# Kernel optimization log

Hardware: AMD Instinct MI355X
Metric: run time of the kernel (lower is better)

## Reference

```python
import jax, jax.numpy as jnp
import numpy as np

N = 50000      # nodes
DEG = 32       # avg degree
E = N * DEG + N  # edges incl. self loops
IN_DIM = 512
H = 4          # heads
D = 128        # hidden per head
SLOPE = 0.2


def setup_inputs() -> dict:
    key = jax.random.key(0)
    ks = jax.random.split(key, 12)
    features = jax.random.normal(ks[0], (N, IN_DIM), dtype=jnp.float32)
    src_r = jax.random.randint(ks[1], (N * DEG,), 0, N)
    dst_r = jax.random.randint(ks[2], (N * DEG,), 0, N)
    loop = jnp.arange(N)
    src = jnp.concatenate([src_r, loop]).astype(jnp.int32)
    dst = jnp.concatenate([dst_r, loop]).astype(jnp.int32)
    ids = jax.random.randint(ks[3], (16,), 0, N)
    s0 = 1.0 / np.sqrt(IN_DIM)
    s1 = 1.0 / np.sqrt(H * D)
    fc_w0 = jax.random.normal(ks[4], (IN_DIM, H * D), dtype=jnp.float32) * s0
    attn_l0 = jax.random.normal(ks[5], (H, D), dtype=jnp.float32) * s1
    attn_r0 = jax.random.normal(ks[6], (H, D), dtype=jnp.float32) * s1
    bias0 = jnp.zeros((H * D,), dtype=jnp.float32)
    fc_w1 = jax.random.normal(ks[7], (H * D, H * D), dtype=jnp.float32) * s1
    attn_l1 = jax.random.normal(ks[8], (H, D), dtype=jnp.float32) * s1
    attn_r1 = jax.random.normal(ks[9], (H, D), dtype=jnp.float32) * s1
    bias1 = jnp.zeros((H * D,), dtype=jnp.float32)
    return dict(features=features, fc_w0=fc_w0, attn_l0=attn_l0, attn_r0=attn_r0,
                bias0=bias0, fc_w1=fc_w1, attn_l1=attn_l1, attn_r1=attn_r1,
                bias1=bias1, src=src, dst=dst, ids=ids)


def gat_layer(h, fc_w, attn_l, attn_r, bias, src, dst, residual):
    ft = (h @ fc_w).reshape(N, H, D)                     # [N,H,D]
    el = jnp.sum(ft * attn_l, axis=-1)                   # [N,H]
    er = jnp.sum(ft * attn_r, axis=-1)                   # [N,H]
    e = jax.nn.leaky_relu(el[src] + er[dst], SLOPE)      # [E,H]
    # edge softmax over incoming edges of each dst node (self-loops guarantee coverage)
    emax = jax.ops.segment_max(e, dst, num_segments=N)   # [N,H]
    ee = jnp.exp(e - emax[dst])
    esum = jax.ops.segment_sum(ee, dst, num_segments=N)  # [N,H]
    alpha = ee / esum[dst]                               # [E,H]
    out = jax.ops.segment_sum(alpha[:, :, None] * ft[src], dst, num_segments=N)  # [N,H,D]
    if residual:
        out = out + h.reshape(N, H, D)                   # res_fc is Identity (in == H*D)
    out = out + bias.reshape(1, H, D)
    out = jax.nn.elu(out)
    return out.reshape(N, H * D)


def reference(features, fc_w0, attn_l0, attn_r0, bias0, fc_w1, attn_l1, attn_r1,
              bias1, src, dst, ids):
    h = gat_layer(features, fc_w0, attn_l0, attn_r0, bias0, src, dst, residual=False)
    h = gat_layer(h, fc_w1, attn_l1, attn_r1, bias1, src, dst, residual=True)
    h = jnp.tanh(h)
    return h[ids]  # [B, H*D] gather per id2node lookup
```

## Files before the change

### kernel.cpp

```cpp
#include <hip/hip_runtime.h>
#include <hip/hip_bf16.h>

typedef short bf16x8 __attribute__((ext_vector_type(8)));
typedef float f32x4 __attribute__((ext_vector_type(4)));

#define HD 512
#define KDIM 512
#define NHEAD 4
#define DHEAD 128
#define C1CAP 1024
#define C2CAP 16384
#define E1CAP 2048
#define E2CAP 32768

struct PassSM {
    unsigned bm[1568];
    int2 eBuf[256];
    int fBuf[256];
    int sid[16];
    int eCnt, fCnt, eBase, fBase, s_c;
};

struct GemmSM {
    __hip_bfloat16 As[128][40];
    __hip_bfloat16 Bs[128][40];
    float pel[2][128];
    float perr[2][128];
};

__device__ int detect_bf16(const unsigned short* f, int* s_c) {
    int c = 0;
#pragma unroll
    for (int k = 0; k < 4; ++k) {
        unsigned short u = f[2 * (threadIdx.x + k * 256)];
        int e = (u >> 7) & 0xFF;
        c += (e >= 96 && e <= 140) ? 1 : 0;
    }
#pragma unroll
    for (int off = 32; off; off >>= 1) c += __shfl_xor(c, off, 64);
    if (threadIdx.x == 0) *s_c = 0;
    __syncthreads();
    if ((threadIdx.x & 63) == 0) atomicAdd(s_c, c);
    __syncthreads();
    int r = (*s_c > 512) ? 1 : 0;
    __syncthreads();
    return r;
}

__device__ __forceinline__ unsigned pk2(float x, float y) {
    __hip_bfloat162 h;
    h.x = __float2bfloat16(x);
    h.y = __float2bfloat16(y);
    return *(unsigned*)&h;
}

template<int MODE>
__device__ void pass_scan(int pid, const int* __restrict__ src,
                          const int* __restrict__ dst, int E, int B,
                          const int* __restrict__ map1g, PassSM& sm,
                          int2* __restrict__ elist, int* ecnt, int ecap,
                          int* __restrict__ cntArr,
                          int* __restrict__ mapm, int* __restrict__ Flist,
                          int* nFr, int fcap) {
    const int t = threadIdx.x;
    const int nq = E >> 2;
    const int gid = pid * 256 + t;
    if (gid < nq) {
        const int4 d4 = ((const int4*)dst)[gid];
        const int dv[4] = {d4.x, d4.y, d4.z, d4.w};
#pragma unroll
        for (int k = 0; k < 4; ++k) {
            const int d = dv[k];
            if ((sm.bm[d >> 5] >> (d & 31)) & 1u) {
                const int e = 4 * gid + k;
                int slot;
                if (MODE == 0) {
                    slot = 0;
                    for (int q = 0; q < B; ++q) if (sm.sid[q] == d) slot = q;
                } else {
                    slot = map1g[d]; if (slot < 0) slot = 0;
                }
                int p = atomicAdd(&cntArr[slot], 1);
                int2 v; v.x = src[e]; v.y = slot | (p << (MODE == 0 ? 4 : 10));
                int pp = atomicAdd(&sm.eCnt, 1);
                if (pp < 256) sm.eBuf[pp] = v;
                else { int q = atomicAdd(ecnt, 1); if (q < ecap) elist[q] = v; }
                const int s = v.x;
                if (atomicCAS(&mapm[s], -1, -2) == -1) {
                    int q = atomicAdd(&sm.fCnt, 1);
                    if (q < 256) sm.fBuf[q] = s;
                    else {
                        int g2 = atomicAdd(nFr, 1);
                        if (g2 < fcap) { Flist[g2] = s; mapm[s] = g2; }
                        else mapm[s] = 0;
                    }
                }
            }
        }
    }
    __syncthreads();
    const int ne = (sm.eCnt < 256) ? sm.eCnt : 256;
    const int nf = (sm.fCnt < 256) ? sm.fCnt : 256;
    if (t == 0 && ne) sm.eBase = atomicAdd(ecnt, ne);
    if (t == 64 && nf) sm.fBase = atomicAdd(nFr, nf);
    __syncthreads();
    for (int i = t; i < ne; i += 256) {
        int pos = sm.eBase + i;
        if (pos < ecap) elist[pos] = sm.eBuf[i];
    }
    for (int i = t; i < nf; i += 256) {
        int q = sm.fBase + i; int s = sm.fBuf[i];
        if (q < fcap) { Flist[q] = s; mapm[s] = q; }
        else mapm[s] = 0;
    }
}

__device__ void gemm_tile(const __hip_bfloat16* __restrict__ A,
                          const int* __restrict__ rowmap,
                          const void* __restrict__ feat, int isbf,
                          const __hip_bfloat16* __restrict__ Bt,
                          __hip_bfloat16* __restrict__ C,
                          const float* __restrict__ al_, const float* __restrict__ ar_,
                          float* __restrict__ el, float* __restrict__ er,
                          int cntv, int m0, int n0, GemmSM& sm) {
    const int t = threadIdx.x;
    const int lane = t & 63, wave = t >> 6;
    const int wm = (wave >> 1) * 64, wn = (wave & 1) * 64;
    const int fr = lane & 15, fk = (lane >> 4) * 8;
    const int r0 = t >> 2;
    const int c0 = (t & 3) * 8;

    int rowsrc[2];
#pragma unroll
    for (int r = 0; r < 2; ++r) {
        int rr = m0 + r * 64 + r0;
        if (rr >= cntv) rr = cntv - 1;
        rowsrc[r] = rowmap ? rowmap[rr] : rr;
    }

    auto loadAB = [&](int kt, uint4 va[2], uint4 vb[2]) {
#pragma unroll
        for (int r = 0; r < 2; ++r) {
            if (!rowmap) {
                va[r] = *(const uint4*)&A[(size_t)rowsrc[r] * KDIM + kt + c0];
            } else if (isbf) {
                va[r] = *(const uint4*)&((const __hip_bfloat16*)feat)[(size_t)rowsrc[r] * KDIM + kt + c0];
            } else {
                const float* fp = (const float*)feat + (size_t)rowsrc[r] * KDIM + kt + c0;
                const float4 f0 = *(const float4*)fp;
                const float4 f1 = *(const float4*)(fp + 4);
                va[r].x = pk2(f0.x, f0.y);
                va[r].y = pk2(f0.z, f0.w);
                va[r].z = pk2(f1.x, f1.y);
                va[r].w = pk2(f1.z, f1.w);
            }
            int row = r * 64 + r0;
            vb[r] = *(const uint4*)&Bt[(size_t)(n0 + row) * KDIM + kt + c0];
        }
    };

    f32x4 acc[4][4];
#pragma unroll
    for (int i = 0; i < 4; ++i)
#pragma unroll
        for (int j = 0; j < 4; ++j)
#pragma unroll
            for (int r = 0; r < 4; ++r) acc[i][j][r] = 0.f;

    uint4 cva[2], cvb[2], nva[2], nvb[2];
    loadAB(0, cva, cvb);
    for (int kt = 0; kt < KDIM; kt += 32) {
#pragma unroll
        for (int r = 0; r < 2; ++r) {
            int row = r * 64 + r0;
            *(uint4*)&sm.As[row][c0] = cva[r];
            *(uint4*)&sm.Bs[row][c0] = cvb[r];
        }
        __syncthreads();
        if (kt + 32 < KDIM) loadAB(kt + 32, nva, nvb);
        bf16x8 af[4], bfr[4];
#pragma unroll
        for (int i = 0; i < 4; ++i) af[i]  = *(const bf16x8*)&sm.As[wm + i * 16 + fr][fk];
#pragma unroll
        for (int j = 0; j < 4; ++j) bfr[j] = *(const bf16x8*)&sm.Bs[wn + j * 16 + fr][fk];
#pragma unroll
        for (int i = 0; i < 4; ++i)
#pragma unroll
            for (int j = 0; j < 4; ++j)
                acc[i][j] = __builtin_amdgcn_mfma_f32_16x16x32_bf16(af[i], bfr[j], acc[i][j], 0, 0, 0);
        __syncthreads();
#pragma unroll
        for (int r = 0; r < 2; ++r) { cva[r] = nva[r]; cvb[r] = nvb[r]; }
    }

    const int cr = (lane >> 4) * 4;
    const int cc = lane & 15;
#pragma unroll
    for (int i = 0; i < 4; ++i)
#pragma unroll
        for (int j = 0; j < 4; ++j)
#pragma unroll
            for (int rg = 0; rg < 4; ++rg) {
                int m = m0 + wm + i * 16 + cr + rg;
                int n = n0 + wn + j * 16 + cc;
                C[(size_t)m * HD + n] = __float2bfloat16(acc[i][j][rg]);
            }

    const int h = n0 >> 7;
    float alv[4], arv[4];
#pragma unroll
    for (int j = 0; j < 4; ++j) {
        alv[j] = al_[h * DHEAD + wn + j * 16 + cc];
        arv[j] = ar_[h * DHEAD + wn + j * 16 + cc];
    }
#pragma unroll
    for (int i = 0; i < 4; ++i)
#pragma unroll
        for (int rg = 0; rg < 4; ++rg) {
            float sl = 0.f, sr = 0.f;
#pragma unroll
            for (int j = 0; j < 4; ++j) {
                float c = acc[i][j][rg];
                sl += c * alv[j];
                sr += c * arv[j];
            }
#pragma unroll
            for (int off = 1; off < 16; off <<= 1) {
                sl += __shfl_xor(sl, off, 16);
                sr += __shfl_xor(sr, off, 16);
            }
            if (cc == 0) {
                int row = wm + i * 16 + cr + rg;
                sm.pel[wn >> 6][row] = sl;
                sm.perr[wn >> 6][row] = sr;
            }
        }
    __syncthreads();
    if (t < 128) {
        int m = m0 + t;
        if (m < cntv) {
            el[m * NHEAD + h] = sm.pel[0][t] + sm.pel[1][t];
            er[m * NHEAD + h] = sm.perr[0][t] + sm.perr[1][t];
        }
    }
    __syncthreads();
}

__global__ __launch_bounds__(256) void prep_pass1_k(
    const void* __restrict__ features,
    const void* __restrict__ W0, const void* __restrict__ W1,
    __hip_bfloat16* __restrict__ Wt0, __hip_bfloat16* __restrict__ Wt1,
    const void* p0, const void* p1, const void* p2,
    const void* p3, const void* p4, const void* p5,
    float* __restrict__ smallc,
    const int* __restrict__ ids, int B, int* __restrict__ mapId,
    const int* __restrict__ src, const int* __restrict__ dst, int E,
    int2* __restrict__ E1l, int* __restrict__ counters,
    int* __restrict__ cnt1, int* __restrict__ map1, int* __restrict__ F1list) {
    __shared__ PassSM sm;
    const int b = blockIdx.x;
    const int t = threadIdx.x;
    if (b < 2048) {
        const int isbf = detect_bf16((const unsigned short*)features, &sm.s_c);
        const void* W = (b < 1024) ? W0 : W1;
        __hip_bfloat16* Wt = (b < 1024) ? Wt0 : Wt1;
        int idx = (b & 1023) * 256 + t;
        int i = idx >> 9, j = idx & 511;
        float v = isbf ? __bfloat162float(((const __hip_bfloat16*)W)[idx])
                       : ((const float*)W)[idx];
        Wt[j * 512 + i] = __float2bfloat16(v);
    } else if (b < 2054) {
        const int isbf = detect_bf16((const unsigned short*)features, &sm.s_c);
        int which = b - 2048;
        const void* p;
        switch (which) {
            case 0: p = p0; break;
            case 1: p = p1; break;
            case 2: p = p2; break;
            case 3: p = p3; break;
            case 4: p = p4; break;
            default: p = p5; break;
        }
#pragma unroll
        for (int r = 0; r < 2; ++r) {
            int e = t + r * 256;
            float v = isbf ? __bfloat162float(((const __hip_bfloat16*)p)[e])
                           : ((const float*)p)[e];
            smallc[which * 512 + e] = v;
        }
    } else if (b == 2054) {
        if (t < B) atomicMax(&mapId[ids[t]], t);
    } else {
        const int pid = b - 2055;
        for (int i = t; i < 1568; i += 256) sm.bm[i] = 0u;
        if (t < 16) sm.sid[t] = (t < B) ? ids[t] : -1;
        if (t == 0) { sm.eCnt = 0; sm.fCnt = 0; }
        __syncthreads();
        if (t < B) { int n = sm.sid[t]; atomicOr(&sm.bm[n >> 5], 1u << (n & 31)); }
        __syncthreads();
        pass_scan<0>(pid, src, dst, E, B, nullptr, sm,
                     E1l, counters + 0, E1CAP, cnt1,
                     map1, F1list, counters + 2, C1CAP);
    }
}

__global__ __launch_bounds__(256) void pass2_k(
    const int* __restrict__ src, const int* __restrict__ dst, int E,
    const int* __restrict__ F1list, int* __restrict__ counters,
    const int* __restrict__ map1,
    int2* __restrict__ E2l, int* __restrict__ cnt2,
    int* __restrict__ map2, int* __restrict__ F2list) {
    __shared__ PassSM sm;
    const int t = threadIdx.x;
    for (int i = t; i < 1568; i += 256) sm.bm[i] = 0u;
    if (t == 0) { sm.eCnt = 0; sm.fCnt = 0; }
    __syncthreads();
    int nf1 = counters[2]; if (nf1 > C1CAP) nf1 = C1CAP;
    for (int i = t; i < nf1; i += 256) {
        int n = F1list[i];
        atomicOr(&sm.bm[n >> 5], 1u << (n & 31));
    }
    __syncthreads();
    pass_scan<1>(blockIdx.x, src, dst, E, 0, map1, sm,
                 E2l, counters + 1, E2CAP, cnt2,
                 map2, F2list, counters + 3, C2CAP);
}

__global__ __launch_bounds__(256) void gemmel_k(
    int do_scatter,
    const int2* __restrict__ E1l, const int2* __restrict__ E2l,
    const int* __restrict__ counters,
    const int* __restrict__ cnt1, const int* __restrict__ cnt2,
    const int* __restrict__ map1, const int* __restrict__ map2,
    int* __restrict__ off1, int* __restrict__ off2,
    int* __restrict__ b1, int* __restrict__ b2,
    const __hip_bfloat16* __restrict__ A, const int* __restrict__ rowmap,
    const void* __restrict__ feat,
    const __hip_bfloat16* __restrict__ Bt, __hip_bfloat16* __restrict__ C,
    const float* __restrict__ al_, const float* __restrict__ ar_,
    float* __restrict__ el, float* __restrict__ er,
    const int* __restrict__ countp, int cap) {
    __shared__ alignas(16) GemmSM sm;
    const int t = threadIdx.x;
    const int bid = blockIdx.x;
    if (do_scatter && bid == 0) {
        int* soff = (int*)&sm;
        int* sc   = soff + 1024;
        int* s1   = sc + 256;
        int c0 = cnt2[t * 4 + 0], c1 = cnt2[t * 4 + 1];
        int c2 = cnt2[t * 4 + 2], c3 = cnt2[t * 4 + 3];
        int tsum = c0 + c1 + c2 + c3;
        sc[t] = tsum;
        __syncthreads();
        for (int off = 1; off < 256; off <<= 1) {
            int x = (t >= off) ? sc[t - off] : 0;
            __syncthreads();
            sc[t] += x;
            __syncthreads();
        }
        int run = sc[t] - tsum;
        int b4 = t * 4;
        off2[b4 + 0] = run; soff[b4 + 0] = run; run += c0;
        off2[b4 + 1] = run; soff[b4 + 1] = run; run += c1;
        off2[b4 + 2] = run; soff[b4 + 2] = run; run += c2;
        off2[b4 + 3] = run; soff[b4 + 3] = run; run += c3;
        if (t == 255) off2[1024] = run;
        if (t == 0) {
            int acc = 0;
            for (int i = 0; i < 16; ++i) { off1[i] = acc; s1[i] = acc; acc += cnt1[i]; }
            off1[16] = acc;
        }
        __syncthreads();
        int n2 = counters[1]; if (n2 > E2CAP) n2 = E2CAP;
        for (int i = t; i < n2; i += 256) {
            int2 v = E2l[i];
            int y = v.y & 1023, p = v.y >> 10;
            int pos = soff[y] + p;
            int r = map2[v.x]; if (r < 0) r = 0;
            if (pos < E2CAP) b2[pos] = r;
        }
        int n1 = counters[0]; if (n1 > E1CAP) n1 = E1CAP;
        for (int i = t; i < n1; i += 256) {
            int2 v = E1l[i];
            int y = v.y & 15, p = v.y >> 4;
            int pos = s1[y] + p;
            int r = map1[v.x]; if (r < 0) r = 0;
            if (pos < E1CAP) b1[pos] = r;
        }
        return;
    }
    int isbf = 0;
    if (rowmap) isbf = detect_bf16((const unsigned short*)feat, (int*)&sm);
    const int nblk = (int)gridDim.x - (do_scatter ? 1 : 0);
    const int start = bid - (do_scatter ? 1 : 0);
    int cntv = *countp; if (cntv > cap) cntv = cap;
    const int nt = ((cntv + 127) >> 7) * 4;
    for (int tile = start; tile < nt; tile += nblk)
        gemm_tile(A, rowmap, feat, isbf, Bt, C, al_, ar_, el, er,
                  cntv, (tile >> 2) * 128, (tile & 3) * 128, sm);
}

__global__ __launch_bounds__(256) void agg1_k(
    const int* __restrict__ off2, const int* __restrict__ b2,
    const int* __restrict__ F1list, const int* __restrict__ map2,
    const int* __restrict__ nF1p,
    const float* __restrict__ el, const float* __restrict__ er,
    const __hip_bfloat16* __restrict__ ftc,
    const float* __restrict__ bias,
    __hip_bfloat16* __restrict__ outc) {
    int b = blockIdx.x;
    if (b >= *nF1p) return;
    int n = F1list[b];
    const int h = threadIdx.x >> 6, lane = threadIdx.x & 63;
    int rn = map2[n]; if (rn < 0) rn = 0;
    float ern = er[rn * NHEAD + h];
    int beg = off2[b], end = off2[b + 1];
    float m = -3.0e38f, l = 0.f, a0 = 0.f, a1 = 0.f;
    int i = beg;
    for (; i + 4 <= end; i += 4) {
        int r4[4]; float ev[4]; __hip_bfloat162 fv[4];
#pragma unroll
        for (int k = 0; k < 4; ++k) {
            int r = b2[i + k]; if ((unsigned)r >= C2CAP) r = 0;
            r4[k] = r;
        }
#pragma unroll
        for (int k = 0; k < 4; ++k) {
            ev[k] = el[r4[k] * NHEAD + h];
            fv[k] = *(const __hip_bfloat162*)&ftc[(size_t)r4[k] * HD + h * DHEAD + lane * 2];
        }
#pragma unroll
        for (int k = 0; k < 4; ++k) {
            float e = ev[k] + ern;
            e = (e >= 0.f) ? e : 0.2f * e;
            float mn = fmaxf(m, e);
            float sc = __expf(m - mn);
            float w  = __expf(e - mn);
            l  = l * sc + w;
            a0 = a0 * sc + w * __bfloat162float(fv[k].x);
            a1 = a1 * sc + w * __bfloat162float(fv[k].y);
            m = mn;
        }
    }
    for (; i < end; ++i) {
        int r2 = b2[i]; if ((unsigned)r2 >= C2CAP) r2 = 0;
        float e = el[r2 * NHEAD + h] + ern;
        e = (e >= 0.f) ? e : 0.2f * e;
        float mn = fmaxf(m, e);
        float sc = __expf(m - mn);
        float w  = __expf(e - mn);
        const __hip_bfloat162 f = *(const __hip_bfloat162*)&ftc[(size_t)r2 * HD + h * DHEAD + lane * 2];
        l  = l * sc + w;
        a0 = a0 * sc + w * __bfloat162float(f.x);
        a1 = a1 * sc + w * __bfloat162float(f.y);
        m = mn;
    }
    float inv = (l > 0.f) ? 1.0f / l : 0.f;
    float o0 = a0 * inv, o1 = a1 * inv;
    const float2 bb = *(const float2*)&bias[h * DHEAD + lane * 2];
    o0 += bb.x; o1 += bb.y;
    o0 = (o0 > 0.f) ? o0 : expm1f(o0);
    o1 = (o1 > 0.f) ? o1 : expm1f(o1);
    __hip_bfloat162 o2;
    o2.x = __float2bfloat16(o0);
    o2.y = __float2bfloat16(o1);
    *(__hip_bfloat162*)&outc[(size_t)b * HD + h * DHEAD + lane * 2] = o2;
}

__global__ __launch_bounds__(256) void agg2_k(
    const int* __restrict__ off1, const int* __restrict__ b1,
    const int* __restrict__ ids, const int* __restrict__ mapId,
    const int* __restrict__ map1,
    const float* __restrict__ el, const float* __restrict__ er,
    const __hip_bfloat16* __restrict__ ftc,
    const __hip_bfloat16* __restrict__ resc,
    const float* __restrict__ bias,
    void* __restrict__ out, const void* __restrict__ features) {
    __shared__ int s_c;
    const int isbf = detect_bf16((const unsigned short*)features, &s_c);
    int b = blockIdx.x;
    int n = ids[b];
    int slot = mapId[n]; if (slot < 0) slot = 0;
    const int h = threadIdx.x >> 6, lane = threadIdx.x & 63;
    int rn = map1[n]; if (rn < 0) rn = 0;
    float ern = er[rn * NHEAD + h];
    int beg = off1[slot], end = off1[slot + 1];
    float m = -3.0e38f, l = 0.f, a0 = 0.f, a1 = 0.f;
    int i = beg;
    for (; i + 4 <= end; i += 4) {
        int r4[4]; float ev[4]; __hip_bfloat162 fv[4];
#pragma unroll
        for (int k = 0; k < 4; ++k) {
            int r = b1[i + k]; if ((unsigned)r >= C1CAP) r = 0;
            r4[k] = r;
        }
#pragma unroll
        for (int k = 0; k < 4; ++k) {
            ev[k] = el[r4[k] * NHEAD + h];
            fv[k] = *(const __hip_bfloat162*)&ftc[(size_t)r4[k] * HD + h * DHEAD + lane * 2];
        }
#pragma unroll
        for (int k = 0; k < 4; ++k) {
            float e = ev[k] + ern;
            e = (e >= 0.f) ? e : 0.2f * e;
            float mn = fmaxf(m, e);
            float sc = __expf(m - mn);
            float w  = __expf(e - mn);
            l  = l * sc + w;
            a0 = a0 * sc + w * __bfloat162float(fv[k].x);
            a1 = a1 * sc + w * __bfloat162float(fv[k].y);
            m = mn;
        }
    }
    for (; i < end; ++i) {
        int r1 = b1[i]; if ((unsigned)r1 >= C1CAP) r1 = 0;
        float e = el[r1 * NHEAD + h] + ern;
        e = (e >= 0.f) ? e : 0.2f * e;
        float mn = fmaxf(m, e);
        float sc = __expf(m - mn);
        float w  = __expf(e - mn);
        const __hip_bfloat162 f = *(const __hip_bfloat162*)&ftc[(size_t)r1 * HD + h * DHEAD + lane * 2];
        l  = l * sc + w;
        a0 = a0 * sc + w * __bfloat162float(f.x);
        a1 = a1 * sc + w * __bfloat162float(f.y);
        m = mn;
    }
    float inv = (l > 0.f) ? 1.0f / l : 0.f;
    float o0 = a0 * inv, o1 = a1 * inv;
    const __hip_bfloat162 rv = *(const __hip_bfloat162*)&resc[(size_t)rn * HD + h * DHEAD + lane * 2];
    o0 += __bfloat162float(rv.x);
    o1 += __bfloat162float(rv.y);
    const float2 bb = *(const float2*)&bias[h * DHEAD + lane * 2];
    o0 += bb.x; o1 += bb.y;
    o0 = (o0 > 0.f) ? o0 : expm1f(o0);
    o1 = (o1 > 0.f) ? o1 : expm1f(o1);
    o0 = tanhf(o0);
    o1 = tanhf(o1);
    size_t oi = (size_t)b * HD + h * DHEAD + lane * 2;
    if (isbf) {
        __hip_bfloat162 o2;
        o2.x = __float2bfloat16(o0);
        o2.y = __float2bfloat16(o1);
        *(__hip_bfloat162*)&((__hip_bfloat16*)out)[oi] = o2;
    } else {
        float2 o2; o2.x = o0; o2.y = o1;
        *(float2*)&((float*)out)[oi] = o2;
    }
}

extern "C" void kernel_launch(void* const* d_in, const int* in_sizes, int n_in,
                              void* d_out, int out_size, void* d_ws, size_t ws_size,
                              hipStream_t stream) {
    const void* features = d_in[0];
    const int* src = (const int*)d_in[9];
    const int* dst = (const int*)d_in[10];
    const int* ids = (const int*)d_in[11];

    const int N = in_sizes[0] / KDIM;
    const int E = in_sizes[9];
    const int B = in_sizes[11];

    char* w = (char*)d_ws;
    auto alloc = [&](size_t bytes) {
        void* p = (void*)w;
        w += (bytes + 255) & ~(size_t)255;
        return p;
    };
    __hip_bfloat16* Wt0 = (__hip_bfloat16*)alloc(512 * 512 * 2);
    __hip_bfloat16* Wt1 = (__hip_bfloat16*)alloc(512 * 512 * 2);
    float* smallc = (float*)alloc(6 * 512 * 4);
    int* maps  = (int*)alloc((size_t)3 * N * 4);
    int* mapId = maps;
    int* map1  = maps + N;
    int* map2  = maps + 2 * N;
    int2* E1l  = (int2*)alloc((size_t)E1CAP * 8);
    int2* E2l  = (int2*)alloc((size_t)E2CAP * 8);
    int* F1list = (int*)alloc(C1CAP * 4);
    int* F2list = (int*)alloc(C2CAP * 4);
    const int zwords = 8 + 16 + 1024;
    int* zmem = (int*)alloc((size_t)zwords * 4);
    int* counters = zmem;
    int* cnt1 = zmem + 8;
    int* cnt2 = cnt1 + 16;
    int* off1 = (int*)alloc(17 * 4);
    int* off2 = (int*)alloc(1025 * 4);
    int* b1   = (int*)alloc(E1CAP * 4);
    int* b2   = (int*)alloc(E2CAP * 4);
    __hip_bfloat16* ft0c = (__hip_bfloat16*)alloc((size_t)C2CAP * HD * 2);
    float* el0 = (float*)alloc((size_t)C2CAP * NHEAD * 4);
    float* er0 = (float*)alloc((size_t)C2CAP * NHEAD * 4);
    __hip_bfloat16* h1c  = (__hip_bfloat16*)alloc((size_t)C1CAP * HD * 2);
    __hip_bfloat16* ft1c = (__hip_bfloat16*)alloc((size_t)C1CAP * HD * 2);
    float* el1 = (float*)alloc((size_t)C1CAP * NHEAD * 4);
    float* er1 = (float*)alloc((size_t)C1CAP * NHEAD * 4);

    hipMemsetAsync(maps, 0xFF, (size_t)3 * N * 4, stream);
    hipMemsetAsync(zmem, 0, (size_t)zwords * 4, stream);

    float* al0c = smallc + 0 * 512;
    float* ar0c = smallc + 1 * 512;
    float* b0c  = smallc + 2 * 512;
    float* al1c = smallc + 3 * 512;
    float* ar1c = smallc + 4 * 512;
    float* b1c  = smallc + 5 * 512;

    const int nblk_scan = (E / 4 + 255) / 256;

    prep_pass1_k<<<2055 + nblk_scan, 256, 0, stream>>>(
        features, d_in[1], d_in[5], Wt0, Wt1,
        d_in[2], d_in[3], d_in[4], d_in[6], d_in[7], d_in[8],
        smallc, ids, B, mapId, src, dst, E,
        E1l, counters, cnt1, map1, F1list);

    pass2_k<<<nblk_scan, 256, 0, stream>>>(src, dst, E, F1list, counters, map1,
                                           E2l, cnt2, map2, F2list);

    gemmel_k<<<513, 256, 0, stream>>>(1, E1l, E2l, counters, cnt1, cnt2,
                                      map1, map2, off1, off2, b1, b2,
                                      nullptr, F2list, features,
                                      Wt0, ft0c, al0c, ar0c, el0, er0,
                                      counters + 3, C2CAP);

    agg1_k<<<C1CAP, 256, 0, stream>>>(off2, b2, F1list, map2, counters + 2,
                                      el0, er0, ft0c, b0c, h1c);

    gemmel_k<<<32, 256, 0, stream>>>(0, E1l, E2l, counters, cnt1, cnt2,
                                     map1, map2, off1, off2, b1, b2,
                                     h1c, nullptr, nullptr,
                                     Wt1, ft1c, al1c, ar1c, el1, er1,
                                     counters + 2, C1CAP);

    agg2_k<<<B, 256, 0, stream>>>(off1, b1, ids, mapId, map1,
                                  el1, er1, ft1c, h1c, b1c,
                                  d_out, features);
}
```

Measured before the change: 353.4 us.

## Tile weight transpose through LDS and pre-gather frontier feature rows

The weight transpose now works on 64x64 tiles staged in shared memory (128 blocks instead of 2048), so reads and writes are both coalesced. Feature rows for the layer-0 frontier are gathered and converted to bf16 by a separate gather kernel into a contiguous buffer, which lets the GEMM read A directly without indirect row mapping or fp32 conversion in its inner loop. This adds one kernel launch and a 16 MB intermediate buffer round trip.

```diff
diff --git a/kernel.cpp b/kernel.cpp
--- a/kernel.cpp
+++ b/kernel.cpp
@@ -21,6 +21,12 @@
     int eCnt, fCnt, eBase, fBase, s_c;
 };
 
+union PrepSM {
+    PassSM pass;
+    float tile[64][65];
+    int s_c;
+};
+
 struct GemmSM {
     __hip_bfloat16 As[128][40];
     __hip_bfloat16 Bs[128][40];
@@ -45,13 +51,6 @@
     int r = (*s_c > 512) ? 1 : 0;
     __syncthreads();
     return r;
-}
-
-__device__ __forceinline__ unsigned pk2(float x, float y) {
-    __hip_bfloat162 h;
-    h.x = __float2bfloat16(x);
-    h.y = __float2bfloat16(y);
-    return *(unsigned*)&h;
 }
 
 template<int MODE>
@@ -116,8 +115,6 @@
 }
 
 __device__ void gemm_tile(const __hip_bfloat16* __restrict__ A,
-                          const int* __restrict__ rowmap,
-                          const void* __restrict__ feat, int isbf,
                           const __hip_bfloat16* __restrict__ Bt,
                           __hip_bfloat16* __restrict__ C,
                           const float* __restrict__ al_, const float* __restrict__ ar_,
@@ -130,30 +127,18 @@
     const int r0 = t >> 2;
     const int c0 = (t & 3) * 8;
 
-    int rowsrc[2];
+    int arow[2];
 #pragma unroll
     for (int r = 0; r < 2; ++r) {
         int rr = m0 + r * 64 + r0;
         if (rr >= cntv) rr = cntv - 1;
-        rowsrc[r] = rowmap ? rowmap[rr] : rr;
+        arow[r] = rr;
     }
 
     auto loadAB = [&](int kt, uint4 va[2], uint4 vb[2]) {
 #pragma unroll
         for (int r = 0; r < 2; ++r) {
-            if (!rowmap) {
-                va[r] = *(const uint4*)&A[(size_t)rowsrc[r] * KDIM + kt + c0];
-            } else if (isbf) {
-                va[r] = *(const uint4*)&((const __hip_bfloat16*)feat)[(size_t)rowsrc[r] * KDIM + kt + c0];
-            } else {
-                const float* fp = (const float*)feat + (size_t)rowsrc[r] * KDIM + kt + c0;
-                const float4 f0 = *(const float4*)fp;
-                const float4 f1 = *(const float4*)(fp + 4);
-                va[r].x = pk2(f0.x, f0.y);
-                va[r].y = pk2(f0.z, f0.w);
-                va[r].z = pk2(f1.x, f1.y);
-                va[r].w = pk2(f1.z, f1.w);
-            }
+            va[r] = *(const uint4*)&A[(size_t)arow[r] * KDIM + kt + c0];
             int row = r * 64 + r0;
             vb[r] = *(const uint4*)&Bt[(size_t)(n0 + row) * KDIM + kt + c0];
         }
@@ -257,21 +242,34 @@
     const int* __restrict__ src, const int* __restrict__ dst, int E,
     int2* __restrict__ E1l, int* __restrict__ counters,
     int* __restrict__ cnt1, int* __restrict__ map1, int* __restrict__ F1list) {
-    __shared__ PassSM sm;
+    __shared__ PrepSM sm;
     const int b = blockIdx.x;
     const int t = threadIdx.x;
-    if (b < 2048) {
+    if (b < 128) {
         const int isbf = detect_bf16((const unsigned short*)features, &sm.s_c);
-        const void* W = (b < 1024) ? W0 : W1;
-        __hip_bfloat16* Wt = (b < 1024) ? Wt0 : Wt1;
-        int idx = (b & 1023) * 256 + t;
-        int i = idx >> 9, j = idx & 511;
-        float v = isbf ? __bfloat162float(((const __hip_bfloat16*)W)[idx])
-                       : ((const float*)W)[idx];
-        Wt[j * 512 + i] = __float2bfloat16(v);
-    } else if (b < 2054) {
+        const int mtx = b >> 6;
+        const int tidx = b & 63;
+        const int i0 = (tidx >> 3) * 64, j0 = (tidx & 7) * 64;
+        const void* W = mtx ? W1 : W0;
+        __hip_bfloat16* Wt = mtx ? Wt1 : Wt0;
+        const int rr = t >> 6, cc = t & 63;
+#pragma unroll
+        for (int it = 0; it < 16; ++it) {
+            int ii = rr + it * 4;
+            size_t idx = (size_t)(i0 + ii) * 512 + j0 + cc;
+            float v = isbf ? __bfloat162float(((const __hip_bfloat16*)W)[idx])
+                           : ((const float*)W)[idx];
+            sm.tile[ii][cc] = v;
+        }
+        __syncthreads();
+#pragma unroll
+        for (int it = 0; it < 16; ++it) {
+            int jj = rr + it * 4;
+            Wt[(size_t)(j0 + jj) * 512 + i0 + cc] = __float2bfloat16(sm.tile[cc][jj]);
+        }
+    } else if (b < 134) {
         const int isbf = detect_bf16((const unsigned short*)features, &sm.s_c);
-        int which = b - 2048;
+        int which = b - 128;
         const void* p;
         switch (which) {
             case 0: p = p0; break;
@@ -288,17 +286,17 @@
                            : ((const float*)p)[e];
             smallc[which * 512 + e] = v;
         }
-    } else if (b == 2054) {
+    } else if (b == 134) {
         if (t < B) atomicMax(&mapId[ids[t]], t);
     } else {
-        const int pid = b - 2055;
-        for (int i = t; i < 1568; i += 256) sm.bm[i] = 0u;
-        if (t < 16) sm.sid[t] = (t < B) ? ids[t] : -1;
-        if (t == 0) { sm.eCnt = 0; sm.fCnt = 0; }
+        const int pid = b - 135;
+        for (int i = t; i < 1568; i += 256) sm.pass.bm[i] = 0u;
+        if (t < 16) sm.pass.sid[t] = (t < B) ? ids[t] : -1;
+        if (t == 0) { sm.pass.eCnt = 0; sm.pass.fCnt = 0; }
         __syncthreads();
-        if (t < B) { int n = sm.sid[t]; atomicOr(&sm.bm[n >> 5], 1u << (n & 31)); }
+        if (t < B) { int n = sm.pass.sid[t]; atomicOr(&sm.pass.bm[n >> 5], 1u << (n & 31)); }
         __syncthreads();
-        pass_scan<0>(pid, src, dst, E, B, nullptr, sm,
+        pass_scan<0>(pid, src, dst, E, B, nullptr, sm.pass,
                      E1l, counters + 0, E1CAP, cnt1,
                      map1, F1list, counters + 2, C1CAP);
     }
@@ -326,6 +324,27 @@
                  map2, F2list, counters + 3, C2CAP);
 }
 
+__global__ __launch_bounds__(256) void gather_k(
+    const void* __restrict__ feat, const int* __restrict__ F2list,
+    const int* __restrict__ nF2p, __hip_bfloat16* __restrict__ Ac) {
+    __shared__ int s_c;
+    const int isbf = detect_bf16((const unsigned short*)feat, &s_c);
+    int cnt = *nF2p; if (cnt > C2CAP) cnt = C2CAP;
+    const int t = threadIdx.x;
+    for (int b = blockIdx.x; b < cnt; b += gridDim.x) {
+        int row = F2list[b];
+        __hip_bfloat162 v;
+        if (isbf) {
+            v = *(const __hip_bfloat162*)&((const __hip_bfloat16*)feat)[(size_t)row * KDIM + t * 2];
+        } else {
+            const float2 f = *(const float2*)&((const float*)feat)[(size_t)row * KDIM + t * 2];
+            v.x = __float2bfloat16(f.x);
+            v.y = __float2bfloat16(f.y);
+        }
+        *(__hip_bfloat162*)&Ac[(size_t)b * KDIM + t * 2] = v;
+    }
+}
+
 __global__ __launch_bounds__(256) void gemmel_k(
     int do_scatter,
     const int2* __restrict__ E1l, const int2* __restrict__ E2l,
@@ -334,8 +353,7 @@
     const int* __restrict__ map1, const int* __restrict__ map2,
     int* __restrict__ off1, int* __restrict__ off2,
     int* __restrict__ b1, int* __restrict__ b2,
-    const __hip_bfloat16* __restrict__ A, const int* __restrict__ rowmap,
-    const void* __restrict__ feat,
+    const __hip_bfloat16* __restrict__ A,
     const __hip_bfloat16* __restrict__ Bt, __hip_bfloat16* __restrict__ C,
     const float* __restrict__ al_, const float* __restrict__ ar_,
     float* __restrict__ el, float* __restrict__ er,
@@ -389,14 +407,12 @@
         }
         return;
     }
-    int isbf = 0;
-    if (rowmap) isbf = detect_bf16((const unsigned short*)feat, (int*)&sm);
     const int nblk = (int)gridDim.x - (do_scatter ? 1 : 0);
     const int start = bid - (do_scatter ? 1 : 0);
     int cntv = *countp; if (cntv > cap) cntv = cap;
     const int nt = ((cntv + 127) >> 7) * 4;
     for (int tile = start; tile < nt; tile += nblk)
-        gemm_tile(A, rowmap, feat, isbf, Bt, C, al_, ar_, el, er,
+        gemm_tile(A, Bt, C, al_, ar_, el, er,
                   cntv, (tile >> 2) * 128, (tile & 3) * 128, sm);
 }
 
@@ -586,6 +602,7 @@
     int* off2 = (int*)alloc(1025 * 4);
     int* b1   = (int*)alloc(E1CAP * 4);
     int* b2   = (int*)alloc(E2CAP * 4);
+    __hip_bfloat16* Ac   = (__hip_bfloat16*)alloc((size_t)C2CAP * KDIM * 2);
     __hip_bfloat16* ft0c = (__hip_bfloat16*)alloc((size_t)C2CAP * HD * 2);
     float* el0 = (float*)alloc((size_t)C2CAP * NHEAD * 4);
     float* er0 = (float*)alloc((size_t)C2CAP * NHEAD * 4);
@@ -606,7 +623,7 @@
 
     const int nblk_scan = (E / 4 + 255) / 256;
 
-    prep_pass1_k<<<2055 + nblk_scan, 256, 0, stream>>>(
+    prep_pass1_k<<<135 + nblk_scan, 256, 0, stream>>>(
         features, d_in[1], d_in[5], Wt0, Wt1,
         d_in[2], d_in[3], d_in[4], d_in[6], d_in[7], d_in[8],
         smallc, ids, B, mapId, src, dst, E,
@@ -615,10 +632,11 @@
     pass2_k<<<nblk_scan, 256, 0, stream>>>(src, dst, E, F1list, counters, map1,
                                            E2l, cnt2, map2, F2list);
 
+    gather_k<<<2048, 256, 0, stream>>>(features, F2list, counters + 3, Ac);
+
     gemmel_k<<<513, 256, 0, stream>>>(1, E1l, E2l, counters, cnt1, cnt2,
                                       map1, map2, off1, off2, b1, b2,
-                                      nullptr, F2list, features,
-                                      Wt0, ft0c, al0c, ar0c, el0, er0,
+                                      Ac, Wt0, ft0c, al0c, ar0c, el0, er0,
                                       counters + 3, C2CAP);
 
     agg1_k<<<C1CAP, 256, 0, stream>>>(off2, b2, F1list, map2, counters + 2,
@@ -626,8 +644,7 @@
 
     gemmel_k<<<32, 256, 0, stream>>>(0, E1l, E2l, counters, cnt1, cnt2,
                                      map1, map2, off1, off2, b1, b2,
-                                     h1c, nullptr, nullptr,
-                                     Wt1, ft1c, al1c, ar1c, el1, er1,
+                                     h1c, Wt1, ft1c, al1c, ar1c, el1, er1,
                                      counters + 2, C1CAP);
 
     agg2_k<<<B, 256, 0, stream>>>(off1, b1, ids, mapId, map1,
```

Measured after the change: 362.8 us. 2.7% more time.
